# Optimization experiments

Hardware: AMD Instinct MI355X
Metric: run time of the kernel (lower is better)

The kernel has to match this reference:

```python
import jax, jax.numpy as jnp
import numpy as np

NUM_GRAPHS = 1024


def gcn_conv(x, src, dst, W, b, num_nodes):
    # PyG GCNConv: x' = D^{-1/2}(A+I)D^{-1/2} X W + b, self-loops added.
    h = x @ W  # [N, out]
    deg = jax.ops.segment_sum(jnp.ones_like(dst, dtype=h.dtype), dst, num_segments=num_nodes)
    dinv = jnp.where(deg > 0, jax.lax.rsqrt(deg), 0.0)
    norm = dinv[src] * dinv[dst]  # [E+N]
    msg = h[src] * norm[:, None]
    out = jax.ops.segment_sum(msg, dst, num_segments=num_nodes)
    return out + b


def setup_inputs() -> dict:
    key = jax.random.key(0)
    ks = jax.random.split(key, 16)
    N, E, F_IN, F_OUT = 100000, 1600000, 128, 256
    x = jax.random.normal(ks[0], (N, F_IN), dtype=jnp.float32)
    edge_index = jax.random.randint(ks[1], (2, E), 0, N, dtype=jnp.int64)
    batch = jnp.sort(jax.random.randint(ks[2], (N,), 0, NUM_GRAPHS, dtype=jnp.int64))

    def glorot(k, shape):
        lim = np.sqrt(6.0 / (shape[0] + shape[1]))
        return jax.random.uniform(k, shape, jnp.float32, -lim, lim)

    return {
        "x": x, "edge_index": edge_index, "batch": batch,
        "W1": glorot(ks[3], (F_IN, 16)), "b1": jnp.zeros((16,), jnp.float32),
        "W2": glorot(ks[4], (16, 32)), "b2": jnp.zeros((32,), jnp.float32),
        "W3": glorot(ks[5], (32, 64)), "b3": jnp.zeros((64,), jnp.float32),
        "L1_w": glorot(ks[6], (64, 256)), "L1_b": jnp.zeros((256,), jnp.float32),
        "L2_w": glorot(ks[7], (256, F_OUT)), "L2_b": jnp.zeros((F_OUT,), jnp.float32),
    }


def reference(x, edge_index, batch, W1, b1, W2, b2, W3, b3, L1_w, L1_b, L2_w, L2_b):
    N = x.shape[0]
    loops = jnp.arange(N, dtype=edge_index.dtype)
    src = jnp.concatenate([edge_index[0], loops])
    dst = jnp.concatenate([edge_index[1], loops])

    h = jax.nn.relu(gcn_conv(x, src, dst, W1, b1, N))
    h = jax.nn.relu(gcn_conv(h, src, dst, W2, b2, N))
    h = jax.nn.relu(gcn_conv(h, src, dst, W3, b3, N))

    pooled = jax.ops.segment_max(h, batch, num_segments=NUM_GRAPHS)  # [G, 64]
    pooled = jnp.where(jnp.isfinite(pooled), pooled, 0.0)  # empty segments -> 0

    z = jax.nn.relu(pooled @ L1_w + L1_b)
    return jax.nn.sigmoid(z @ L2_w + L2_b)
```

## Files before the change

kernel.cpp:

```cpp
#include <hip/hip_runtime.h>
#include <hip/hip_fp16.h>
#include <math.h>

#define NG 1024
#define EPB 2048
#define EPB_BIN 4096

static inline int cdiv_i(long long a, int b) { return (int)((a + b - 1) / b); }

union H8 { uint4 u; __half2 h[4]; };

__device__ inline void h8_to_f(uint4 uu, float* f) {
    H8 v; v.u = uu;
#pragma unroll
    for (int k = 0; k < 4; ++k) {
        float2 t = __half22float2(v.h[k]);
        f[2 * k] = t.x; f[2 * k + 1] = t.y;
    }
}
__device__ inline uint4 f_to_h8(const float* f) {
    H8 v;
#pragma unroll
    for (int k = 0; k < 4; ++k) v.h[k] = __floats2half2_rn(f[2 * k], f[2 * k + 1]);
    return v.u;
}

__global__ void zero_init(int* __restrict__ bcnt, unsigned* __restrict__ pooled) {
    int t = blockIdx.x * 256 + threadIdx.x;
    if (t < 256) bcnt[t] = 0;
    if (t < NG * 64) pooled[t] = 0;
}


__global__ void bucket_count(const int* __restrict__ dst, int* __restrict__ bcnt, int E) {
    __shared__ int h[256];
    int t = threadIdx.x;
    h[t] = 0;
    __syncthreads();
    int e0 = blockIdx.x * EPB;
#pragma unroll 4
    for (int k = 0; k < EPB / 256; ++k) {
        int e = e0 + k * 256 + t;
        if (e < E) atomicAdd(&h[dst[e] >> 9], 1);
    }
    __syncthreads();
    if (h[t] > 0) atomicAdd(&bcnt[t], h[t]);
}

__global__ void bucket_scan(const int* __restrict__ bcnt, int* __restrict__ bktbase,
                            int* __restrict__ bktcur, int* __restrict__ rowptr,
                            int NBKT, int N) {
    __shared__ int s[256];
    int t = threadIdx.x;
    int v = (t < NBKT) ? bcnt[t] : 0;
    s[t] = v;
    __syncthreads();
    for (int off = 1; off < 256; off <<= 1) {
        int u = (t >= off) ? s[t - off] : 0;
        __syncthreads();
        s[t] += u;
        __syncthreads();
    }
    int excl = s[t] - v;
    if (t < NBKT) { bktbase[t] = excl; bktcur[t] = excl; }
    if (t == 255) { bktbase[NBKT] = s[255]; rowptr[N] = s[255]; }
}

__global__ void bin_edges(const int* __restrict__ src, const int* __restrict__ dst,
                          int* __restrict__ bktcur, unsigned* __restrict__ binned, int E) {
    __shared__ int hist[256];
    __shared__ int sc[256];
    __shared__ int lofs[256];
    __shared__ int gbase[256];
    __shared__ int lcur[256];
    __shared__ unsigned stage[EPB_BIN];
    __shared__ int gaddr[EPB_BIN];
    int t = threadIdx.x;
    hist[t] = 0;
    __syncthreads();
    int e0 = blockIdx.x * EPB_BIN;
    int ne = E - e0; if (ne > EPB_BIN) ne = EPB_BIN;
    int myd[EPB_BIN / 256];
    int mys[EPB_BIN / 256];
#pragma unroll
    for (int k = 0; k < EPB_BIN / 256; ++k) {
        int e = e0 + k * 256 + t;
        if (e < E) {
            int d = dst[e];
            myd[k] = d;
            atomicAdd(&hist[d >> 9], 1);
        } else {
            myd[k] = -1;
        }
    }
#pragma unroll
    for (int k = 0; k < EPB_BIN / 256; ++k) {
        int e = e0 + k * 256 + t;
        mys[k] = (e < E) ? src[e] : 0;
    }
    __syncthreads();
    int v = hist[t];
    sc[t] = v;
    __syncthreads();
    for (int off = 1; off < 256; off <<= 1) {
        int u = (t >= off) ? sc[t - off] : 0;
        __syncthreads();
        sc[t] += u;
        __syncthreads();
    }
    lofs[t] = sc[t] - v;
    lcur[t] = sc[t] - v;
    if (v > 0) gbase[t] = atomicAdd(&bktcur[t], v);
    __syncthreads();
#pragma unroll
    for (int k = 0; k < EPB_BIN / 256; ++k) {
        int d = myd[k];
        if (d >= 0) {
            int b = d >> 9;
            int r = atomicAdd(&lcur[b], 1);
            stage[r] = ((unsigned)(d & 511) << 23) | (unsigned)mys[k];
            gaddr[r] = gbase[b] + (r - lofs[b]);
        }
    }
    __syncthreads();
    for (int j = t; j < ne; j += 256) binned[gaddr[j]] = stage[j];
}

__global__ void bucket_build(const int* __restrict__ bktbase, const unsigned* __restrict__ binned,
                             int* __restrict__ rowptr, float* __restrict__ dinv,
                             int* __restrict__ csr_src, int N) {
    __shared__ int degl[512];
    __shared__ int s[512];
    __shared__ int rp[512];
    __shared__ int cur[512];
    int t = threadIdx.x;
    int n0 = blockIdx.x << 9;
    degl[t] = 0;
    cur[t] = 0;
    __syncthreads();
    int base = bktbase[blockIdx.x], end = bktbase[blockIdx.x + 1];
    for (int j = base + t; j < end; j += 512) atomicAdd(&degl[binned[j] >> 23], 1);
    __syncthreads();
    int d = degl[t];
    s[t] = d;
    __syncthreads();
    for (int off = 1; off < 512; off <<= 1) {
        int u = (t >= off) ? s[t - off] : 0;
        __syncthreads();
        s[t] += u;
        __syncthreads();
    }
    rp[t] = base + s[t] - d;
    int i = n0 + t;
    if (i < N) {
        rowptr[i] = rp[t];
        dinv[i] = rsqrtf((float)(d + 1));
    }
    __syncthreads();
    for (int j = base + t; j < end; j += 512) {
        unsigned v = binned[j];
        int li = v >> 23;
        int slot = rp[li] + atomicAdd(&cur[li], 1);
        csr_src[slot] = (int)(v & 0x7FFFFFu);
    }
}

__global__ void gemm1(const float* __restrict__ x, const float* __restrict__ dinv,
                      const float* __restrict__ W, uint4* __restrict__ t1, int N) {
    __shared__ float Wl[128 * 16];
    int t = threadIdx.x;
    for (int k = t; k < 128 * 16; k += 256) Wl[k] = W[k];
    __syncthreads();
    int i = blockIdx.x * 256 + t;
    if (i >= N) return;
    const float4* x4 = (const float4*)(x + (size_t)i * 128);
    const float4* W4 = (const float4*)Wl;
    float4 a[4];
#pragma unroll
    for (int c = 0; c < 4; ++c) a[c] = make_float4(0.f, 0.f, 0.f, 0.f);
#pragma unroll 4
    for (int k4 = 0; k4 < 32; ++k4) {
        float4 v = x4[k4];
#pragma unroll
        for (int kk = 0; kk < 4; ++kk) {
            float xk = (kk == 0) ? v.x : (kk == 1) ? v.y : (kk == 2) ? v.z : v.w;
            const float4* Wr = W4 + (k4 * 4 + kk) * 4;
#pragma unroll
            for (int c = 0; c < 4; ++c) {
                float4 w = Wr[c];
                a[c].x += xk * w.x; a[c].y += xk * w.y;
                a[c].z += xk * w.z; a[c].w += xk * w.w;
            }
        }
    }
    float di = dinv[i];
    float f[16];
#pragma unroll
    for (int c = 0; c < 4; ++c) {
        f[4 * c + 0] = di * a[c].x; f[4 * c + 1] = di * a[c].y;
        f[4 * c + 2] = di * a[c].z; f[4 * c + 3] = di * a[c].w;
    }
    t1[(size_t)i * 2]     = f_to_h8(f);
    t1[(size_t)i * 2 + 1] = f_to_h8(f + 8);
}

template <bool EPI>
__global__ void gather16(const int* __restrict__ rowptr, const int* __restrict__ csr_src,
                         const uint4* __restrict__ hs, const float* __restrict__ dinv,
                         const float* __restrict__ b, uint4* __restrict__ out, int N) {
    int tid = blockIdx.x * 256 + threadIdx.x;
    int i = tid >> 1, c = tid & 1;
    if (i >= N) return;
    float acc[8];
    h8_to_f(hs[(size_t)i * 2 + c], acc);
    int j = rowptr[i], end = rowptr[i + 1];
    for (; j < end; ++j) {
        int s = csr_src[j];
        float v[8];
        h8_to_f(hs[(size_t)s * 2 + c], v);
#pragma unroll
        for (int k = 0; k < 8; ++k) acc[k] += v[k];
    }
    if (EPI) {
        float di = dinv[i];
#pragma unroll
        for (int k = 0; k < 8; ++k) acc[k] = di * fmaxf(di * acc[k] + b[c * 8 + k], 0.f);
    }
    out[(size_t)i * 2 + c] = f_to_h8(acc);
}

__global__ void gather_gemm2(const int* __restrict__ rowptr, const int* __restrict__ csr_src,
                             const uint4* __restrict__ p1, const float* __restrict__ dinv,
                             const float* __restrict__ W, const float* __restrict__ b,
                             uint4* __restrict__ p2a, uint4* __restrict__ p2b, int N) {
    __shared__ float Wl[16 * 32];
    __shared__ float bl[32];
    int t = threadIdx.x;
    for (int k = t; k < 16 * 32; k += 256) Wl[k] = W[k];
    if (t < 32) bl[t] = b[t];
    __syncthreads();
    int i = blockIdx.x * 256 + t;
    if (i >= N) return;
    float f[16];
    h8_to_f(p1[(size_t)i * 2], f);
    h8_to_f(p1[(size_t)i * 2 + 1], f + 8);
    int j = rowptr[i], end = rowptr[i + 1];
    for (; j < end; ++j) {
        int s = csr_src[j];
        float v[16];
        h8_to_f(p1[(size_t)s * 2], v);
        h8_to_f(p1[(size_t)s * 2 + 1], v + 8);
#pragma unroll
        for (int k = 0; k < 16; ++k) f[k] += v[k];
    }
    const float4* W4 = (const float4*)Wl;
    float4 a[8];
#pragma unroll
    for (int c = 0; c < 8; ++c) a[c] = make_float4(0.f, 0.f, 0.f, 0.f);
#pragma unroll
    for (int k = 0; k < 16; ++k) {
        float xk = f[k];
        const float4* Wr = W4 + k * 8;
#pragma unroll
        for (int c = 0; c < 8; ++c) {
            float4 w = Wr[c];
            a[c].x += xk * w.x; a[c].y += xk * w.y;
            a[c].z += xk * w.z; a[c].w += xk * w.w;
        }
    }
    float di = dinv[i];
    float o[32];
#pragma unroll
    for (int c = 0; c < 8; ++c) {
        o[4 * c + 0] = di * fmaxf(di * a[c].x + bl[4 * c + 0], 0.f);
        o[4 * c + 1] = di * fmaxf(di * a[c].y + bl[4 * c + 1], 0.f);
        o[4 * c + 2] = di * fmaxf(di * a[c].z + bl[4 * c + 2], 0.f);
        o[4 * c + 3] = di * fmaxf(di * a[c].w + bl[4 * c + 3], 0.f);
    }
    p2a[(size_t)i * 2]     = f_to_h8(o);
    p2a[(size_t)i * 2 + 1] = f_to_h8(o + 8);
    p2b[(size_t)i * 2]     = f_to_h8(o + 16);
    p2b[(size_t)i * 2 + 1] = f_to_h8(o + 24);
}

__global__ void gemm3_pool(const uint4* __restrict__ g3a, const uint4* __restrict__ g3b,
                           const float* __restrict__ dinv, const float* __restrict__ W,
                           const float* __restrict__ b, const int* __restrict__ batch,
                           unsigned* __restrict__ pooled, int N) {
    __shared__ float Wl[32 * 64];
    __shared__ float bl[64];
    __shared__ float pl[128][65];
    __shared__ int bt[128];
    int t = threadIdx.x;
    for (int k = t; k < 32 * 64; k += 256) Wl[k] = W[k];
    if (t < 64) bl[t] = b[t];
    int i0 = blockIdx.x * 128;
    if (t < 128) {
        int i = i0 + t;
        bt[t] = (i < N) ? batch[i] : -1;
    }
    __syncthreads();
    int il = t & 127, c = t >> 7;
    int i = i0 + il;
    if (i < N) {
        float f[32];
        h8_to_f(g3a[(size_t)i * 2], f);
        h8_to_f(g3a[(size_t)i * 2 + 1], f + 8);
        h8_to_f(g3b[(size_t)i * 2], f + 16);
        h8_to_f(g3b[(size_t)i * 2 + 1], f + 24);
        const float4* W4 = (const float4*)Wl;
        float4 a[8];
#pragma unroll
        for (int cc = 0; cc < 8; ++cc) a[cc] = make_float4(0.f, 0.f, 0.f, 0.f);
#pragma unroll 4
        for (int k = 0; k < 32; ++k) {
            float xk = f[k];
            const float4* Wr = W4 + k * 16 + c * 8;
#pragma unroll
            for (int cc = 0; cc < 8; ++cc) {
                float4 w = Wr[cc];
                a[cc].x += xk * w.x; a[cc].y += xk * w.y;
                a[cc].z += xk * w.z; a[cc].w += xk * w.w;
            }
        }
        float di = dinv[i];
        int fb = c * 32;
#pragma unroll
        for (int cc = 0; cc < 8; ++cc) {
            pl[il][fb + 4 * cc + 0] = fmaxf(di * a[cc].x + bl[fb + 4 * cc + 0], 0.f);
            pl[il][fb + 4 * cc + 1] = fmaxf(di * a[cc].y + bl[fb + 4 * cc + 1], 0.f);
            pl[il][fb + 4 * cc + 2] = fmaxf(di * a[cc].z + bl[fb + 4 * cc + 2], 0.f);
            pl[il][fb + 4 * cc + 3] = fmaxf(di * a[cc].w + bl[fb + 4 * cc + 3], 0.f);
        }
    }
    __syncthreads();
    int f = t & 63, q = t >> 6;
    int prevb = -1;
    float run = 0.f;
    for (int k = 0; k < 32; ++k) {
        int il2 = q * 32 + k;
        int bg = bt[il2];
        if (bg < 0) break;
        float v = pl[il2][f];
        if (bg != prevb) {
            if (prevb >= 0) atomicMax(&pooled[prevb * 64 + f], __float_as_uint(run));
            prevb = bg;
            run = v;
        } else {
            run = fmaxf(run, v);
        }
    }
    if (prevb >= 0) atomicMax(&pooled[prevb * 64 + f], __float_as_uint(run));
}

__global__ void head(const float* __restrict__ pooled, const float* __restrict__ w1,
                     const float* __restrict__ bb1, const float* __restrict__ w2,
                     const float* __restrict__ bb2, float* __restrict__ out) {
    __shared__ float p[64];
    __shared__ float z[256];
    int g = blockIdx.x, t = threadIdx.x;
    if (t < 64) p[t] = pooled[g * 64 + t];
    __syncthreads();
    float s = bb1[t];
#pragma unroll
    for (int k = 0; k < 64; ++k) s += p[k] * w1[k * 256 + t];
    z[t] = fmaxf(s, 0.f);
    __syncthreads();
    float s2 = bb2[t];
#pragma unroll 8
    for (int k = 0; k < 256; ++k) s2 += z[k] * w2[k * 256 + t];
    out[g * 256 + t] = 1.f / (1.f + expf(-s2));
}

extern "C" void kernel_launch(void* const* d_in, const int* in_sizes, int n_in,
                              void* d_out, int out_size, void* d_ws, size_t ws_size,
                              hipStream_t stream) {
    const float* x   = (const float*)d_in[0];
    const int* ei    = (const int*)d_in[1];
    const int* batch = (const int*)d_in[2];
    const float* W1  = (const float*)d_in[3];
    const float* b1  = (const float*)d_in[4];
    const float* W2  = (const float*)d_in[5];
    const float* b2  = (const float*)d_in[6];
    const float* W3  = (const float*)d_in[7];
    const float* b3  = (const float*)d_in[8];
    const float* L1w = (const float*)d_in[9];
    const float* L1b = (const float*)d_in[10];
    const float* L2w = (const float*)d_in[11];
    const float* L2b = (const float*)d_in[12];

    const int N = in_sizes[0] / 128;
    const int E = in_sizes[1] / 2;
    const int* srcp = ei;
    const int* dstp = ei + E;
    const int NB = cdiv_i(N, 256);
    const int NBKT = cdiv_i(N, 512);

    char* w = (char*)d_ws;
    auto carve = [&](size_t bytes) { char* p = w; w += (bytes + 15) & ~(size_t)15; return p; };
    int*   bcnt    = (int*)carve(256 * 4);
    int*   bktbase = (int*)carve(257 * 4);
    int*   bktcur  = (int*)carve(256 * 4);
    int*   rowptr  = (int*)carve((size_t)(N + 1) * 4);
    int*   csr_src = (int*)carve((size_t)E * 4);
    float* dinv    = (float*)carve((size_t)N * 4);
    uint4* t1      = (uint4*)carve((size_t)N * 32);
    uint4* p1      = (uint4*)carve((size_t)N * 32);
    uint4* p2a     = (uint4*)carve((size_t)N * 32);
    uint4* p2b     = (uint4*)carve((size_t)N * 32);
    uint4* g3a     = (uint4*)carve((size_t)N * 32);
    uint4* g3b     = (uint4*)carve((size_t)N * 32);
    unsigned* binned = (unsigned*)carve((size_t)E * 4);
    unsigned* pooled = (unsigned*)carve((size_t)NG * 64 * 4);

    zero_init<<<cdiv_i(NG * 64, 256), 256, 0, stream>>>(bcnt, pooled);

    bucket_count<<<cdiv_i(E, EPB), 256, 0, stream>>>(dstp, bcnt, E);
    bucket_scan<<<1, 256, 0, stream>>>(bcnt, bktbase, bktcur, rowptr, NBKT, N);
    bin_edges<<<cdiv_i(E, EPB_BIN), 256, 0, stream>>>(srcp, dstp, bktcur, binned, E);
    bucket_build<<<NBKT, 512, 0, stream>>>(bktbase, binned, rowptr, dinv, csr_src, N);

    const int GG = cdiv_i((long long)N * 2, 256);

    gemm1<<<NB, 256, 0, stream>>>(x, dinv, W1, t1, N);
    gather16<true><<<GG, 256, 0, stream>>>(rowptr, csr_src, t1, dinv, b1, p1, N);

    gather_gemm2<<<NB, 256, 0, stream>>>(rowptr, csr_src, p1, dinv, W2, b2, p2a, p2b, N);

    gather16<false><<<GG, 256, 0, stream>>>(rowptr, csr_src, p2a, nullptr, nullptr, g3a, N);
    gather16<false><<<GG, 256, 0, stream>>>(rowptr, csr_src, p2b, nullptr, nullptr, g3b, N);
    gemm3_pool<<<cdiv_i(N, 128), 256, 0, stream>>>(g3a, g3b, dinv, W3, b3, batch, pooled, N);

    head<<<NG, 256, 0, stream>>>((const float*)pooled, L1w, L1b, L2w, L2b, (float*)d_out);
}
```

Measured before the change: 209.7 us.

## Fuse layer-3 gather into GEMM3/pool kernel, unroll gathers, batch head by four graphs

Moves the two layer-3 neighbour-gather kernels into the GEMM3+max-pool kernel. Each thread now gathers a 16-feature half-row straight from p2a or p2b and stages it in shared memory, which removes two launches and the g3a/g3b intermediate write and read. All gather loops are unrolled by two edges so each thread has more loads in flight. The head kernel now handles four graphs per block so each weight load is reused four times. The fused kernel uses more shared memory per block, which may lower occupancy, and its per-thread 16-wide gather loads less evenly than the old 8-wide split.

```diff
diff --git a/kernel.cpp b/kernel.cpp
--- a/kernel.cpp
+++ b/kernel.cpp
@@ -204,28 +204,35 @@
     t1[(size_t)i * 2 + 1] = f_to_h8(f + 8);
 }
 
-template <bool EPI>
-__global__ void gather16(const int* __restrict__ rowptr, const int* __restrict__ csr_src,
-                         const uint4* __restrict__ hs, const float* __restrict__ dinv,
-                         const float* __restrict__ b, uint4* __restrict__ out, int N) {
+__global__ void gather16_epi(const int* __restrict__ rowptr, const int* __restrict__ csr_src,
+                             const uint4* __restrict__ hs, const float* __restrict__ dinv,
+                             const float* __restrict__ b, uint4* __restrict__ out, int N) {
     int tid = blockIdx.x * 256 + threadIdx.x;
     int i = tid >> 1, c = tid & 1;
     if (i >= N) return;
     float acc[8];
     h8_to_f(hs[(size_t)i * 2 + c], acc);
     int j = rowptr[i], end = rowptr[i + 1];
-    for (; j < end; ++j) {
-        int s = csr_src[j];
-        float v[8];
-        h8_to_f(hs[(size_t)s * 2 + c], v);
-#pragma unroll
-        for (int k = 0; k < 8; ++k) acc[k] += v[k];
-    }
-    if (EPI) {
-        float di = dinv[i];
-#pragma unroll
-        for (int k = 0; k < 8; ++k) acc[k] = di * fmaxf(di * acc[k] + b[c * 8 + k], 0.f);
-    }
+    for (; j + 1 < end; j += 2) {
+        int s0 = csr_src[j], s1 = csr_src[j + 1];
+        uint4 u0 = hs[(size_t)s0 * 2 + c];
+        uint4 u1 = hs[(size_t)s1 * 2 + c];
+        float v0[8], v1[8];
+        h8_to_f(u0, v0);
+        h8_to_f(u1, v1);
+#pragma unroll
+        for (int k = 0; k < 8; ++k) acc[k] += v0[k] + v1[k];
+    }
+    if (j < end) {
+        int s0 = csr_src[j];
+        float v0[8];
+        h8_to_f(hs[(size_t)s0 * 2 + c], v0);
+#pragma unroll
+        for (int k = 0; k < 8; ++k) acc[k] += v0[k];
+    }
+    float di = dinv[i];
+#pragma unroll
+    for (int k = 0; k < 8; ++k) acc[k] = di * fmaxf(di * acc[k] + b[c * 8 + k], 0.f);
     out[(size_t)i * 2 + c] = f_to_h8(acc);
 }
 
@@ -245,11 +252,21 @@
     h8_to_f(p1[(size_t)i * 2], f);
     h8_to_f(p1[(size_t)i * 2 + 1], f + 8);
     int j = rowptr[i], end = rowptr[i + 1];
-    for (; j < end; ++j) {
-        int s = csr_src[j];
+    for (; j + 1 < end; j += 2) {
+        int s0 = csr_src[j], s1 = csr_src[j + 1];
+        uint4 a0 = p1[(size_t)s0 * 2], a1 = p1[(size_t)s0 * 2 + 1];
+        uint4 b0 = p1[(size_t)s1 * 2], b1 = p1[(size_t)s1 * 2 + 1];
+        float v[16], u[16];
+        h8_to_f(a0, v); h8_to_f(a1, v + 8);
+        h8_to_f(b0, u); h8_to_f(b1, u + 8);
+#pragma unroll
+        for (int k = 0; k < 16; ++k) f[k] += v[k] + u[k];
+    }
+    if (j < end) {
+        int s0 = csr_src[j];
         float v[16];
-        h8_to_f(p1[(size_t)s * 2], v);
-        h8_to_f(p1[(size_t)s * 2 + 1], v + 8);
+        h8_to_f(p1[(size_t)s0 * 2], v);
+        h8_to_f(p1[(size_t)s0 * 2 + 1], v + 8);
 #pragma unroll
         for (int k = 0; k < 16; ++k) f[k] += v[k];
     }
@@ -283,12 +300,14 @@
     p2b[(size_t)i * 2 + 1] = f_to_h8(o + 24);
 }
 
-__global__ void gemm3_pool(const uint4* __restrict__ g3a, const uint4* __restrict__ g3b,
-                           const float* __restrict__ dinv, const float* __restrict__ W,
-                           const float* __restrict__ b, const int* __restrict__ batch,
-                           unsigned* __restrict__ pooled, int N) {
+__global__ void gather_gemm3_pool(const int* __restrict__ rowptr, const int* __restrict__ csr_src,
+                                  const uint4* __restrict__ p2a, const uint4* __restrict__ p2b,
+                                  const float* __restrict__ dinv, const float* __restrict__ W,
+                                  const float* __restrict__ b, const int* __restrict__ batch,
+                                  unsigned* __restrict__ pooled, int N) {
     __shared__ float Wl[32 * 64];
     __shared__ float bl[64];
+    __shared__ float fl[128][33];
     __shared__ float pl[128][65];
     __shared__ int bt[128];
     int t = threadIdx.x;
@@ -299,22 +318,45 @@
         int i = i0 + t;
         bt[t] = (i < N) ? batch[i] : -1;
     }
-    __syncthreads();
     int il = t & 127, c = t >> 7;
     int i = i0 + il;
     if (i < N) {
-        float f[32];
-        h8_to_f(g3a[(size_t)i * 2], f);
-        h8_to_f(g3a[(size_t)i * 2 + 1], f + 8);
-        h8_to_f(g3b[(size_t)i * 2], f + 16);
-        h8_to_f(g3b[(size_t)i * 2 + 1], f + 24);
+        const uint4* P = c ? p2b : p2a;
+        float acc[16];
+        uint4 s0 = P[(size_t)i * 2], s1 = P[(size_t)i * 2 + 1];
+        h8_to_f(s0, acc);
+        h8_to_f(s1, acc + 8);
+        int j = rowptr[i], end = rowptr[i + 1];
+        for (; j + 1 < end; j += 2) {
+            int n0 = csr_src[j], n1 = csr_src[j + 1];
+            uint4 a0 = P[(size_t)n0 * 2], a1 = P[(size_t)n0 * 2 + 1];
+            uint4 b0 = P[(size_t)n1 * 2], b1 = P[(size_t)n1 * 2 + 1];
+            float v[16], u[16];
+            h8_to_f(a0, v); h8_to_f(a1, v + 8);
+            h8_to_f(b0, u); h8_to_f(b1, u + 8);
+#pragma unroll
+            for (int k = 0; k < 16; ++k) acc[k] += v[k] + u[k];
+        }
+        if (j < end) {
+            int n0 = csr_src[j];
+            float v[16];
+            h8_to_f(P[(size_t)n0 * 2], v);
+            h8_to_f(P[(size_t)n0 * 2 + 1], v + 8);
+#pragma unroll
+            for (int k = 0; k < 16; ++k) acc[k] += v[k];
+        }
+#pragma unroll
+        for (int k = 0; k < 16; ++k) fl[il][c * 16 + k] = acc[k];
+    }
+    __syncthreads();
+    if (i < N) {
         const float4* W4 = (const float4*)Wl;
         float4 a[8];
 #pragma unroll
         for (int cc = 0; cc < 8; ++cc) a[cc] = make_float4(0.f, 0.f, 0.f, 0.f);
 #pragma unroll 4
         for (int k = 0; k < 32; ++k) {
-            float xk = f[k];
+            float xk = fl[il][k];
             const float4* Wr = W4 + k * 16 + c * 8;
 #pragma unroll
             for (int cc = 0; cc < 8; ++cc) {
@@ -353,23 +395,36 @@
     if (prevb >= 0) atomicMax(&pooled[prevb * 64 + f], __float_as_uint(run));
 }
 
-__global__ void head(const float* __restrict__ pooled, const float* __restrict__ w1,
-                     const float* __restrict__ bb1, const float* __restrict__ w2,
-                     const float* __restrict__ bb2, float* __restrict__ out) {
-    __shared__ float p[64];
-    __shared__ float z[256];
-    int g = blockIdx.x, t = threadIdx.x;
-    if (t < 64) p[t] = pooled[g * 64 + t];
-    __syncthreads();
-    float s = bb1[t];
-#pragma unroll
-    for (int k = 0; k < 64; ++k) s += p[k] * w1[k * 256 + t];
-    z[t] = fmaxf(s, 0.f);
-    __syncthreads();
-    float s2 = bb2[t];
-#pragma unroll 8
-    for (int k = 0; k < 256; ++k) s2 += z[k] * w2[k * 256 + t];
-    out[g * 256 + t] = 1.f / (1.f + expf(-s2));
+__global__ void head4(const float* __restrict__ pooled, const float* __restrict__ w1,
+                      const float* __restrict__ bb1, const float* __restrict__ w2,
+                      const float* __restrict__ bb2, float* __restrict__ out) {
+    __shared__ float p[4][64];
+    __shared__ float z[4][256];
+    int g0 = blockIdx.x * 4, t = threadIdx.x;
+    p[t >> 6][t & 63] = pooled[(g0 + (t >> 6)) * 64 + (t & 63)];
+    __syncthreads();
+    float s[4];
+#pragma unroll
+    for (int q = 0; q < 4; ++q) s[q] = bb1[t];
+    for (int k = 0; k < 64; ++k) {
+        float w = w1[k * 256 + t];
+#pragma unroll
+        for (int q = 0; q < 4; ++q) s[q] += p[q][k] * w;
+    }
+#pragma unroll
+    for (int q = 0; q < 4; ++q) z[q][t] = fmaxf(s[q], 0.f);
+    __syncthreads();
+    float s2[4];
+#pragma unroll
+    for (int q = 0; q < 4; ++q) s2[q] = bb2[t];
+#pragma unroll 4
+    for (int k = 0; k < 256; ++k) {
+        float w = w2[k * 256 + t];
+#pragma unroll
+        for (int q = 0; q < 4; ++q) s2[q] += z[q][k] * w;
+    }
+#pragma unroll
+    for (int q = 0; q < 4; ++q) out[(g0 + q) * 256 + t] = 1.f / (1.f + expf(-s2[q]));
 }
 
 extern "C" void kernel_launch(void* const* d_in, const int* in_sizes, int n_in,
@@ -408,8 +463,6 @@
     uint4* p1      = (uint4*)carve((size_t)N * 32);
     uint4* p2a     = (uint4*)carve((size_t)N * 32);
     uint4* p2b     = (uint4*)carve((size_t)N * 32);
-    uint4* g3a     = (uint4*)carve((size_t)N * 32);
-    uint4* g3b     = (uint4*)carve((size_t)N * 32);
     unsigned* binned = (unsigned*)carve((size_t)E * 4);
     unsigned* pooled = (unsigned*)carve((size_t)NG * 64 * 4);
 
@@ -423,13 +476,12 @@
     const int GG = cdiv_i((long long)N * 2, 256);
 
     gemm1<<<NB, 256, 0, stream>>>(x, dinv, W1, t1, N);
-    gather16<true><<<GG, 256, 0, stream>>>(rowptr, csr_src, t1, dinv, b1, p1, N);
+    gather16_epi<<<GG, 256, 0, stream>>>(rowptr, csr_src, t1, dinv, b1, p1, N);
 
     gather_gemm2<<<NB, 256, 0, stream>>>(rowptr, csr_src, p1, dinv, W2, b2, p2a, p2b, N);
 
-    gather16<false><<<GG, 256, 0, stream>>>(rowptr, csr_src, p2a, nullptr, nullptr, g3a, N);
-    gather16<false><<<GG, 256, 0, stream>>>(rowptr, csr_src, p2b, nullptr, nullptr, g3b, N);
-    gemm3_pool<<<cdiv_i(N, 128), 256, 0, stream>>>(g3a, g3b, dinv, W3, b3, batch, pooled, N);
-
-    head<<<NG, 256, 0, stream>>>((const float*)pooled, L1w, L1b, L2w, L2b, (float*)d_out);
-}
+    gather_gemm3_pool<<<cdiv_i(N, 128), 256, 0, stream>>>(
+        rowptr, csr_src, p2a, p2b, dinv, W3, b3, batch, pooled, N);
+
+    head4<<<NG / 4, 256, 0, stream>>>((const float*)pooled, L1w, L1b, L2w, L2b, (float*)d_out);
+}
```

Result: faster. 204.4 us (-2.5%).
